# Kernel optimization log

Measured on AMD Instinct MI355X. Metric: run time of the kernel, lower is better.

## Reference

```python
import jax, jax.numpy as jnp
import numpy as np
import math

B, S, D, H = 2, 2048, 1024, 16
DH = D // H  # head_dim = 64


def setup_inputs() -> dict:
    key = jax.random.key(0)
    k0, k1, k2 = jax.random.split(key, 3)
    x = jax.random.normal(k0, (B, S, D), dtype=jnp.float32)
    Wi = jax.random.normal(k1, (3 * D, D), dtype=jnp.float32) * 0.02  # torch (out,in) layout
    bi = jnp.zeros((3 * D,), dtype=jnp.float32)
    Wo = jax.random.normal(k2, (D, D), dtype=jnp.float32) * 0.02
    bo = jnp.zeros((D,), dtype=jnp.float32)
    return {"x": x, "Wi": Wi, "bi": bi, "Wo": Wo, "bo": bo, "causal_mask": 1}


def reference(x, Wi, bi, Wo, bo, causal_mask):
    b, s, d = x.shape
    # fused QKV projection: nn.Linear applies x @ W.T + b
    qkv = x @ Wi.T + bi                      # (b, s, 3d)
    q, k, v = jnp.split(qkv, 3, axis=-1)
    # (b, s, d) -> (b, h, s, dh)
    def to_heads(t):
        return t.reshape(b, s, H, DH).transpose(0, 2, 1, 3)
    q, k, v = to_heads(q), to_heads(k), to_heads(v)
    scores = jnp.einsum("bhqd,bhkd->bhqk", q, k)  # (b, h, s, s)
    if causal_mask:
        # mask strictly-upper triangle with -inf BEFORE scaling (as in source; -inf unaffected)
        tri = jnp.triu(jnp.ones((s, s), dtype=bool), k=1)
        scores = jnp.where(tri, -jnp.inf, scores)
    scores = scores / math.sqrt(DH)
    weight = jax.nn.softmax(scores, axis=-1)
    out = jnp.einsum("bhqk,bhkd->bhqd", weight, v)  # (b, h, s, dh)
    out = out.transpose(0, 2, 1, 3).reshape(b, s, d)
    return out @ Wo.T + bo
```

## Files before the change

### kernel.cpp

```cpp
#include <hip/hip_runtime.h>
#include <hip/hip_bf16.h>
#include <stdint.h>

#define B_    2
#define S_    2048
#define D_    1024
#define H_    16
#define DH_   64
#define MTOT  (B_*S_)
#define NQKV  (3*D_)

typedef __attribute__((ext_vector_type(8))) short  bf16x8;
typedef __attribute__((ext_vector_type(4))) short  bf16x4;
typedef __attribute__((ext_vector_type(4))) float  f32x4;
typedef __attribute__((ext_vector_type(8))) unsigned short u16x8;
typedef unsigned short ushort_t;

__device__ __forceinline__ ushort_t f2bf(float f) {
  union { float f; unsigned int i; } v; v.f = f;
  unsigned int r = v.i + 0x7FFF + ((v.i >> 16) & 1);
  return (ushort_t)(r >> 16);
}

__device__ __forceinline__ unsigned cvt_pk_bf16(float lo, float hi) {
  unsigned r;
  asm("v_cvt_pk_bf16_f32 %0, %1, %2" : "=v"(r) : "v"(lo), "v"(hi));
  return r;
}

__device__ __forceinline__ float fexp2(float x) {
  float r;
  asm("v_exp_f32 %0, %1" : "=v"(r) : "v"(x));
  return r;
}

#if __has_builtin(__builtin_amdgcn_mfma_f32_16x16x16_bf16)
__device__ __forceinline__ f32x4 mfma16(bf16x4 a, bf16x4 b, f32x4 c) {
  return __builtin_amdgcn_mfma_f32_16x16x16_bf16(a, b, c, 0, 0, 0);
}
#elif __has_builtin(__builtin_amdgcn_mfma_f32_16x16x16bf16_1k)
__device__ __forceinline__ f32x4 mfma16(bf16x4 a, bf16x4 b, f32x4 c) {
  return __builtin_amdgcn_mfma_f32_16x16x16bf16_1k(a, b, c, 0, 0, 0);
}
#else
__device__ __forceinline__ f32x4 mfma16(bf16x4 a, bf16x4 b, f32x4 c) {
  asm volatile("v_mfma_f32_16x16x16_bf16 %0, %1, %2, %0"
               : "+v"(c) : "v"(a), "v"(b));
  return c;
}
#endif

__device__ __forceinline__ void gl_lds16(const ushort_t* g, ushort_t* l) {
  __builtin_amdgcn_global_load_lds(
      (const __attribute__((address_space(1))) unsigned int*)g,
      (__attribute__((address_space(3))) unsigned int*)l, 16, 0, 0);
}

#define CVN1 (MTOT*D_/8)
#define CVN2 (NQKV*D_/8)
#define CVN3 (D_*D_/8)
__global__ __launch_bounds__(256) void cvt_all(
    const float* __restrict__ x, const float* __restrict__ Wi, const float* __restrict__ Wo,
    ushort_t* __restrict__ xb, ushort_t* __restrict__ Wib, ushort_t* __restrict__ Wob) {
  int i = blockIdx.x * blockDim.x + threadIdx.x;
  const float* src; ushort_t* dst; int k;
  if (i < CVN1)            { src = x;  dst = xb;  k = i; }
  else if (i < CVN1+CVN2)  { src = Wi; dst = Wib; k = i - CVN1; }
  else                     { src = Wo; dst = Wob; k = i - CVN1 - CVN2; }
  const float4* s4 = (const float4*)src;
  float4 a = s4[2*k], b = s4[2*k+1];
  u16x8 o;
  o[0]=f2bf(a.x); o[1]=f2bf(a.y); o[2]=f2bf(a.z); o[3]=f2bf(a.w);
  o[4]=f2bf(b.x); o[5]=f2bf(b.y); o[6]=f2bf(b.z); o[7]=f2bf(b.w);
  ((u16x8*)dst)[k] = o;
}

#define BKQ 32
#define BKO 64
#define QSCALE 0.18033688011112042f
__global__ __launch_bounds__(256) void gemm_qkv(
    const ushort_t* __restrict__ Abf, const ushort_t* __restrict__ Bbf,
    const float* __restrict__ bias,
    ushort_t* __restrict__ qb, ushort_t* __restrict__ kb, ushort_t* __restrict__ vb) {
  __shared__ __align__(16) ushort_t Al[2][128*BKQ];
  __shared__ __align__(16) ushort_t Bl[2][128*BKQ];
  int tid = threadIdx.x;
  int w = tid >> 6, lane = tid & 63;
  int wrow = (w >> 1) * 64, wcol = (w & 1) * 64;
  int bid = blockIdx.y * 24 + blockIdx.x;
  int swz = (bid & 7) * 96 + (bid >> 3);
  int m0 = (swz / 24) * 128, n0 = (swz % 24) * 128;
  const int K = D_;
  const int nt = K / BKQ;

  auto stageg = [&](int t, int buf) {
    int k0 = t * BKQ;
    #pragma unroll
    for (int it = 0; it < 2; ++it) {
      int c = it*256 + tid;
      int row = c >> 2, cc = c & 3;
      int lbase = (it*256 + w*64) * 8;
      gl_lds16(Abf + (size_t)(m0+row)*K + k0 + cc*8, &Al[buf][lbase]);
      gl_lds16(Bbf + (size_t)(n0+row)*K + k0 + cc*8, &Bl[buf][lbase]);
    }
  };

  f32x4 zero = {0.f, 0.f, 0.f, 0.f};
  f32x4 acc[4][4];
  for (int i=0;i<4;i++) for (int j=0;j<4;j++) acc[i][j] = zero;

  stageg(0, 0);
  asm volatile("s_waitcnt vmcnt(0)" ::: "memory");
  __builtin_amdgcn_s_barrier();

  for (int t = 0; t < nt; ++t) {
    int cur = t & 1;
    if (t + 1 < nt) stageg(t + 1, cur ^ 1);
    int kof = (lane >> 4) * 8;
    bf16x8 af[4], bfr[4];
    for (int i=0;i<4;i++) af[i]  = *(const bf16x8*)(&Al[cur][(wrow + i*16 + (lane&15))*BKQ + kof]);
    for (int j=0;j<4;j++) bfr[j] = *(const bf16x8*)(&Bl[cur][(wcol + j*16 + (lane&15))*BKQ + kof]);
    for (int i=0;i<4;i++)
      for (int j=0;j<4;j++)
        acc[i][j] = __builtin_amdgcn_mfma_f32_16x16x32_bf16(af[i], bfr[j], acc[i][j], 0, 0, 0);
    asm volatile("s_waitcnt vmcnt(0)" ::: "memory");
    __builtin_amdgcn_s_barrier();
  }
  for (int i=0;i<4;i++)
    for (int j=0;j<4;j++)
      for (int r=0;r<4;r++) {
        int gm = m0 + wrow + i*16 + (lane>>4)*4 + r;
        int gn = n0 + wcol + j*16 + (lane&15);
        float v = acc[i][j][r] + bias[gn];
        int b = gm >> 11, s = gm & (S_-1);
        int sect = gn >> 10, hn = gn & (D_-1);
        int hh = hn >> 6, d = hn & 63;
        size_t idx = (((size_t)(b*H_ + hh))*S_ + s)*DH_ + d;
        if (sect == 0) v *= QSCALE;
        ushort_t val = f2bf(v);
        if (sect == 0) qb[idx] = val;
        else if (sect == 1) kb[idx] = val;
        else vb[idx] = val;
      }
}

__global__ __launch_bounds__(256) void transpose_v(
    const ushort_t* __restrict__ vb, ushort_t* __restrict__ vtb) {
  __shared__ ushort_t T[64*72];
  int bh = blockIdx.y;
  int s0 = blockIdx.x * 64;
  int tid = threadIdx.x;
  const ushort_t* src = vb + (size_t)bh * S_ * DH_;
  ushort_t* dst = vtb + (size_t)bh * DH_ * S_;
  for (int it = 0; it < 2; ++it) {
    int c = it*256 + tid;
    int row = c >> 3, cc = c & 7;
    *(uint4*)&T[row*72 + cc*8] = *(const uint4*)(src + (size_t)(s0+row)*DH_ + cc*8);
  }
  __syncthreads();
  for (int it = 0; it < 2; ++it) {
    int c = it*256 + tid;
    int d = c >> 3, sc = c & 7;
    u16x8 o;
    #pragma unroll
    for (int e = 0; e < 8; ++e) o[e] = T[(sc*8+e)*72 + d];
    *(u16x8*)(dst + (size_t)d*S_ + s0 + sc*8) = o;
  }
}

#define KVB 64
#define DTHR 8.0f
__global__ __launch_bounds__(256) void attn_fwd(
    const ushort_t* __restrict__ qb, const ushort_t* __restrict__ kb,
    const ushort_t* __restrict__ vtb, ushort_t* __restrict__ attnb,
    const int* __restrict__ causal) {
  int wg = blockIdx.x;
  int xcd = wg & 7;
  int j = wg >> 3;
  int v = j >> 5;
  int u = j & 31;
  int a = u >> 2;
  int qi = v*8 + ((v & 1) ? (7 - a) : a);
  int qblk = 31 - qi;
  int bh = (u & 3) * 8 + xcd;
  int b = bh >> 4, h = bh & 15;
  int tid = threadIdx.x, w = tid >> 6, lane = tid & 63;
  int g = lane >> 4, q16 = lane & 15;
  const ushort_t* qh  = qb  + (size_t)bh * S_ * DH_;
  const ushort_t* kh  = kb  + (size_t)bh * S_ * DH_;
  const ushort_t* vth = vtb + (size_t)bh * DH_ * S_;
  __shared__ __align__(16) ushort_t Kl[2][KVB*64];
  __shared__ __align__(16) ushort_t Vtl[2][64*KVB];
  bool use_causal = (causal[0] != 0);

  int nkv = use_causal ? (qblk + 1) : (S_/KVB);
  int qw = qblk*64 + w*16;

  bf16x8 qc0 = *(const bf16x8*)(qh + (size_t)(qw + q16)*DH_ +  0 + g*8);
  bf16x8 qc1 = *(const bf16x8*)(qh + (size_t)(qw + q16)*DH_ + 32 + g*8);

  int c0 = tid, c1 = tid + 256;
  int r0 = c0 >> 3, sw0 = ((c0 & 7) ^ (r0 & 7)) * 8;
  int r1 = c1 >> 3, sw1 = ((c1 & 7) ^ (r1 & 7)) * 8;
  const ushort_t* kp0 = kh + r0*DH_ + sw0;
  const ushort_t* kp1 = kh + r1*DH_ + sw1;
  const ushort_t* vp0 = vth + (size_t)r0*S_ + sw0;
  const ushort_t* vp1 = vth + (size_t)r1*S_ + sw1;

  auto stage = [&](int t, int buf) {
    size_t kadv = (size_t)(t*KVB) * DH_;
    int vadv = t*KVB;
    gl_lds16(kp0 + kadv, &Kl[buf][c0*8]);
    gl_lds16(kp1 + kadv, &Kl[buf][c1*8]);
    gl_lds16(vp0 + vadv, &Vtl[buf][c0*8]);
    gl_lds16(vp1 + vadv, &Vtl[buf][c1*8]);
  };

  f32x4 zero = {0.f,0.f,0.f,0.f};
  f32x4 o[4];
  #pragma unroll
  for (int dt=0;dt<4;dt++) o[dt] = zero;
  float mrun = -1e30f, lrun = 0.f;

  stage(0, 0);
  asm volatile("s_waitcnt vmcnt(0)" ::: "memory");
  __builtin_amdgcn_s_barrier();

  for (int it = 0; it < nkv; ++it) {
    int cur = it & 1;
    int kvbase = it * KVB;
    if (it + 1 < nkv) stage(it + 1, cur ^ 1);

    f32x4 sacc[4];
    #pragma unroll
    for (int j2=0;j2<4;j2++) sacc[j2] = zero;
    #pragma unroll
    for (int kk=0;kk<2;kk++) {
      bf16x8 qf = kk ? qc1 : qc0;
      #pragma unroll
      for (int j2=0;j2<4;j2++) {
        int row = j2*16 + q16;
        int slot = (kk*4 + g) ^ (row & 7);
        bf16x8 kf = *(const bf16x8*)(&Kl[cur][row*64 + slot*8]);
        sacc[j2] = __builtin_amdgcn_mfma_f32_16x16x32_bf16(kf, qf, sacc[j2], 0, 0, 0);
      }
    }
    if (use_causal && kvbase + KVB - 1 > qw) {
      int qd = qw + q16 - kvbase;
      #pragma unroll
      for (int j2=0;j2<4;j2++)
        #pragma unroll
        for (int r=0;r<4;r++)
          if (16*j2 + 4*g + r > qd) sacc[j2][r] = -1e30f;
    }
    float m0v = fmaxf(fmaxf(sacc[0][0], sacc[0][1]), fmaxf(sacc[0][2], sacc[0][3]));
    float m1v = fmaxf(fmaxf(sacc[1][0], sacc[1][1]), fmaxf(sacc[1][2], sacc[1][3]));
    float m2v = fmaxf(fmaxf(sacc[2][0], sacc[2][1]), fmaxf(sacc[2][2], sacc[2][3]));
    float m3v = fmaxf(fmaxf(sacc[3][0], sacc[3][1]), fmaxf(sacc[3][2], sacc[3][3]));
    float mx = fmaxf(fmaxf(m0v, m1v), fmaxf(m2v, m3v));
    mx = fmaxf(mx, __shfl_xor(mx, 16, 64));
    mx = fmaxf(mx, __shfl_xor(mx, 32, 64));
    if (!__all(mx - mrun <= DTHR)) {
      float mnew = fmaxf(mrun, mx);
      float alpha = fexp2(mrun - mnew);
      lrun *= alpha;
      float av0 = __shfl(alpha, 4*g + 0, 64);
      float av1 = __shfl(alpha, 4*g + 1, 64);
      float av2 = __shfl(alpha, 4*g + 2, 64);
      float av3 = __shfl(alpha, 4*g + 3, 64);
      #pragma unroll
      for (int dt=0;dt<4;dt++) {
        o[dt][0] *= av0; o[dt][1] *= av1; o[dt][2] *= av2; o[dt][3] *= av3;
      }
      mrun = mnew;
    }
    float p[4][4];
    float rs = 0.f;
    #pragma unroll
    for (int j2=0;j2<4;j2++)
      #pragma unroll
      for (int r=0;r<4;r++) {
        p[j2][r] = fexp2(sacc[j2][r] - mrun);
        rs += p[j2][r];
      }
    rs += __shfl_xor(rs, 16, 64);
    rs += __shfl_xor(rs, 32, 64);
    lrun += rs;
    #pragma unroll
    for (int s=0;s<4;s++) {
      union { unsigned u2[2]; bf16x4 v2; } pk;
      pk.u2[0] = cvt_pk_bf16(p[s][0], p[s][1]);
      pk.u2[1] = cvt_pk_bf16(p[s][2], p[s][3]);
      int E = 16*s + 4*g;
      #pragma unroll
      for (int dt=0;dt<4;dt++) {
        int row = dt*16 + q16;
        int off = row*64 + ((E >> 3) ^ (row & 7))*8 + (E & 7);
        bf16x4 vf = *(const bf16x4*)(&Vtl[cur][off]);
        o[dt] = mfma16(pk.v2, vf, o[dt]);
      }
    }
    asm volatile("s_waitcnt vmcnt(0)" ::: "memory");
    __builtin_amdgcn_s_barrier();
  }
  float li0 = 1.f / __shfl(lrun, 4*g + 0, 64);
  float li1 = 1.f / __shfl(lrun, 4*g + 1, 64);
  float li2 = 1.f / __shfl(lrun, 4*g + 2, 64);
  float li3 = 1.f / __shfl(lrun, 4*g + 3, 64);
  #pragma unroll
  for (int r=0;r<4;r++) {
    float li = (r==0)?li0:(r==1)?li1:(r==2)?li2:li3;
    int q = qw + 4*g + r;
    #pragma unroll
    for (int dt=0;dt<4;dt++) {
      int d = dt*16 + q16;
      attnb[((size_t)(b*S_ + q))*D_ + h*DH_ + d] = f2bf(o[dt][r] * li);
    }
  }
}

__global__ __launch_bounds__(512) void gemm_out(
    const ushort_t* __restrict__ Abf, const ushort_t* __restrict__ Bbf,
    const float* __restrict__ bias, float* __restrict__ out) {
  __shared__ __align__(16) ushort_t Al[2][128*BKO];
  __shared__ __align__(16) ushort_t Bl[2][128*BKO];
  int tid = threadIdx.x;
  int w = tid >> 6, lane = tid & 63;
  int g = lane >> 4, q16 = lane & 15;
  int wrow = (w >> 2) * 64, wcol = (w & 3) * 32;
  int m0 = blockIdx.y * 128, n0 = blockIdx.x * 128;
  const int K = D_;
  const int nt = K / BKO;

  auto stageg = [&](int t, int buf) {
    int k0 = t * BKO;
    #pragma unroll
    for (int it = 0; it < 2; ++it) {
      int c = it*512 + tid;
      int row = c >> 3, scc = ((c & 7) ^ (row & 7)) * 8;
      gl_lds16(Abf + (size_t)(m0+row)*K + k0 + scc, &Al[buf][c*8]);
      gl_lds16(Bbf + (size_t)(n0+row)*K + k0 + scc, &Bl[buf][c*8]);
    }
  };

  f32x4 zero = {0.f,0.f,0.f,0.f};
  f32x4 acc[4][2];
  for (int i=0;i<4;i++) for (int j=0;j<2;j++) acc[i][j] = zero;

  stageg(0, 0);
  asm volatile("s_waitcnt vmcnt(0)" ::: "memory");
  __builtin_amdgcn_s_barrier();

  for (int t = 0; t < nt; ++t) {
    int cur = t & 1;
    if (t + 1 < nt) stageg(t + 1, cur ^ 1);
    #pragma unroll
    for (int kk = 0; kk < 2; ++kk) {
      bf16x8 af[4], bfr[2];
      #pragma unroll
      for (int i=0;i<4;i++) {
        int row = wrow + i*16 + q16;
        int slot = ((kk*4 + g) ^ (row & 7)) * 8;
        af[i] = *(const bf16x8*)(&Al[cur][row*BKO + slot]);
      }
      #pragma unroll
      for (int j=0;j<2;j++) {
        int row = wcol + j*16 + q16;
        int slot = ((kk*4 + g) ^ (row & 7)) * 8;
        bfr[j] = *(const bf16x8*)(&Bl[cur][row*BKO + slot]);
      }
      #pragma unroll
      for (int i=0;i<4;i++)
        #pragma unroll
        for (int j=0;j<2;j++)
          acc[i][j] = __builtin_amdgcn_mfma_f32_16x16x32_bf16(af[i], bfr[j], acc[i][j], 0, 0, 0);
    }
    asm volatile("s_waitcnt vmcnt(0)" ::: "memory");
    __builtin_amdgcn_s_barrier();
  }
  #pragma unroll
  for (int i=0;i<4;i++)
    #pragma unroll
    for (int j=0;j<2;j++)
      #pragma unroll
      for (int r=0;r<4;r++) {
        int gm = m0 + wrow + i*16 + g*4 + r;
        int gn = n0 + wcol + j*16 + q16;
        out[(size_t)gm*D_ + gn] = acc[i][j][r] + bias[gn];
      }
}

extern "C" void kernel_launch(void* const* d_in, const int* in_sizes, int n_in,
                              void* d_out, int out_size, void* d_ws, size_t ws_size,
                              hipStream_t stream) {
  const float* x  = (const float*)d_in[0];
  const float* Wi = (const float*)d_in[1];
  const float* bi = (const float*)d_in[2];
  const float* Wo = (const float*)d_in[3];
  const float* bo = (const float*)d_in[4];
  const int* causal = (const int*)d_in[5];
  float* out = (float*)d_out;

  ushort_t* xb   = (ushort_t*)d_ws;
  ushort_t* Wib  = xb  + (size_t)MTOT*D_;
  ushort_t* Wob  = Wib + (size_t)NQKV*D_;
  ushort_t* qbuf = Wob + (size_t)D_*D_;
  ushort_t* kbuf = qbuf + (size_t)B_*H_*S_*DH_;
  ushort_t* vbuf = kbuf + (size_t)B_*H_*S_*DH_;
  ushort_t* attnb = vbuf + (size_t)B_*H_*S_*DH_;
  ushort_t* vtb  = xb;

  int ntot = CVN1 + CVN2 + CVN3;
  cvt_all<<<(ntot+255)/256, 256, 0, stream>>>(x, Wi, Wo, xb, Wib, Wob);

  gemm_qkv<<<dim3(NQKV/128, MTOT/128), 256, 0, stream>>>(xb, Wib, bi, qbuf, kbuf, vbuf);
  transpose_v<<<dim3(S_/64, B_*H_), 256, 0, stream>>>(vbuf, vtb);
  attn_fwd<<<1024, 256, 0, stream>>>(qbuf, kbuf, vtb, attnb, causal);
  gemm_out<<<dim3(D_/128, MTOT/128), 512, 0, stream>>>(attnb, Wob, bo, out);
}
```

Baseline: 119.6 us.

## Process two 16-row query tiles per wave in attention to reuse K/V fragments

```diff
diff --git a/kernel.cpp b/kernel.cpp
--- a/kernel.cpp
+++ b/kernel.cpp
@@ -170,7 +170,7 @@
 
 #define KVB 64
 #define DTHR 8.0f
-__global__ __launch_bounds__(256) void attn_fwd(
+__global__ __launch_bounds__(128) void attn_fwd(
     const ushort_t* __restrict__ qb, const ushort_t* __restrict__ kb,
     const ushort_t* __restrict__ vtb, ushort_t* __restrict__ attnb,
     const int* __restrict__ causal) {
@@ -194,33 +194,41 @@
   bool use_causal = (causal[0] != 0);
 
   int nkv = use_causal ? (qblk + 1) : (S_/KVB);
-  int qw = qblk*64 + w*16;
-
-  bf16x8 qc0 = *(const bf16x8*)(qh + (size_t)(qw + q16)*DH_ +  0 + g*8);
-  bf16x8 qc1 = *(const bf16x8*)(qh + (size_t)(qw + q16)*DH_ + 32 + g*8);
-
-  int c0 = tid, c1 = tid + 256;
-  int r0 = c0 >> 3, sw0 = ((c0 & 7) ^ (r0 & 7)) * 8;
-  int r1 = c1 >> 3, sw1 = ((c1 & 7) ^ (r1 & 7)) * 8;
-  const ushort_t* kp0 = kh + r0*DH_ + sw0;
-  const ushort_t* kp1 = kh + r1*DH_ + sw1;
-  const ushort_t* vp0 = vth + (size_t)r0*S_ + sw0;
-  const ushort_t* vp1 = vth + (size_t)r1*S_ + sw1;
-
+  int qw = qblk*64 + w*32;
+
+  bf16x8 qc[2][2];
+  #pragma unroll
+  for (int qt=0; qt<2; ++qt)
+    #pragma unroll
+    for (int kk=0; kk<2; ++kk)
+      qc[qt][kk] = *(const bf16x8*)(qh + (size_t)(qw + qt*16 + q16)*DH_ + kk*32 + g*8);
+
+  const ushort_t* kp[4]; const ushort_t* vp[4]; int ldo[4];
+  #pragma unroll
+  for (int k2=0;k2<4;k2++) {
+    int c = tid + k2*128;
+    int row = c >> 3, sw = ((c & 7) ^ (row & 7)) * 8;
+    kp[k2] = kh + row*DH_ + sw;
+    vp[k2] = vth + (size_t)row*S_ + sw;
+    ldo[k2] = c*8;
+  }
   auto stage = [&](int t, int buf) {
     size_t kadv = (size_t)(t*KVB) * DH_;
     int vadv = t*KVB;
-    gl_lds16(kp0 + kadv, &Kl[buf][c0*8]);
-    gl_lds16(kp1 + kadv, &Kl[buf][c1*8]);
-    gl_lds16(vp0 + vadv, &Vtl[buf][c0*8]);
-    gl_lds16(vp1 + vadv, &Vtl[buf][c1*8]);
+    #pragma unroll
+    for (int k2=0;k2<4;k2++) {
+      gl_lds16(kp[k2] + kadv, &Kl[buf][ldo[k2]]);
+      gl_lds16(vp[k2] + vadv, &Vtl[buf][ldo[k2]]);
+    }
   };
 
   f32x4 zero = {0.f,0.f,0.f,0.f};
-  f32x4 o[4];
+  f32x4 o[2][4];
   #pragma unroll
-  for (int dt=0;dt<4;dt++) o[dt] = zero;
-  float mrun = -1e30f, lrun = 0.f;
+  for (int qt=0;qt<2;qt++)
+    #pragma unroll
+    for (int dt=0;dt<4;dt++) o[qt][dt] = zero;
+  float mrun[2] = {-1e30f, -1e30f}, lrun[2] = {0.f, 0.f};
 
   stage(0, 0);
   asm volatile("s_waitcnt vmcnt(0)" ::: "memory");
@@ -231,90 +239,110 @@
     int kvbase = it * KVB;
     if (it + 1 < nkv) stage(it + 1, cur ^ 1);
 
-    f32x4 sacc[4];
-    #pragma unroll
-    for (int j2=0;j2<4;j2++) sacc[j2] = zero;
-    #pragma unroll
-    for (int kk=0;kk<2;kk++) {
-      bf16x8 qf = kk ? qc1 : qc0;
+    bf16x8 kf[2][4];
+    #pragma unroll
+    for (int kk=0;kk<2;kk++)
       #pragma unroll
       for (int j2=0;j2<4;j2++) {
         int row = j2*16 + q16;
         int slot = (kk*4 + g) ^ (row & 7);
-        bf16x8 kf = *(const bf16x8*)(&Kl[cur][row*64 + slot*8]);
-        sacc[j2] = __builtin_amdgcn_mfma_f32_16x16x32_bf16(kf, qf, sacc[j2], 0, 0, 0);
-      }
-    }
-    if (use_causal && kvbase + KVB - 1 > qw) {
-      int qd = qw + q16 - kvbase;
+        kf[kk][j2] = *(const bf16x8*)(&Kl[cur][row*64 + slot*8]);
+      }
+    f32x4 sacc[2][4];
+    #pragma unroll
+    for (int qt=0;qt<2;qt++)
+      #pragma unroll
+      for (int j2=0;j2<4;j2++) sacc[qt][j2] = zero;
+    #pragma unroll
+    for (int qt=0;qt<2;qt++)
+      #pragma unroll
+      for (int kk=0;kk<2;kk++)
+        #pragma unroll
+        for (int j2=0;j2<4;j2++)
+          sacc[qt][j2] = __builtin_amdgcn_mfma_f32_16x16x32_bf16(kf[kk][j2], qc[qt][kk], sacc[qt][j2], 0, 0, 0);
+
+    bf16x4 pkv[2][4];
+    #pragma unroll
+    for (int qt=0;qt<2;qt++) {
+      if (use_causal && kvbase + KVB - 1 > qw + qt*16) {
+        int qd = qw + qt*16 + q16 - kvbase;
+        #pragma unroll
+        for (int j2=0;j2<4;j2++)
+          #pragma unroll
+          for (int r=0;r<4;r++)
+            if (16*j2 + 4*g + r > qd) sacc[qt][j2][r] = -1e30f;
+      }
+      float m0v = fmaxf(fmaxf(sacc[qt][0][0], sacc[qt][0][1]), fmaxf(sacc[qt][0][2], sacc[qt][0][3]));
+      float m1v = fmaxf(fmaxf(sacc[qt][1][0], sacc[qt][1][1]), fmaxf(sacc[qt][1][2], sacc[qt][1][3]));
+      float m2v = fmaxf(fmaxf(sacc[qt][2][0], sacc[qt][2][1]), fmaxf(sacc[qt][2][2], sacc[qt][2][3]));
+      float m3v = fmaxf(fmaxf(sacc[qt][3][0], sacc[qt][3][1]), fmaxf(sacc[qt][3][2], sacc[qt][3][3]));
+      float mx = fmaxf(fmaxf(m0v, m1v), fmaxf(m2v, m3v));
+      mx = fmaxf(mx, __shfl_xor(mx, 16, 64));
+      mx = fmaxf(mx, __shfl_xor(mx, 32, 64));
+      if (!__all(mx - mrun[qt] <= DTHR)) {
+        float mnew = fmaxf(mrun[qt], mx);
+        float alpha = fexp2(mrun[qt] - mnew);
+        lrun[qt] *= alpha;
+        float av0 = __shfl(alpha, 4*g + 0, 64);
+        float av1 = __shfl(alpha, 4*g + 1, 64);
+        float av2 = __shfl(alpha, 4*g + 2, 64);
+        float av3 = __shfl(alpha, 4*g + 3, 64);
+        #pragma unroll
+        for (int dt=0;dt<4;dt++) {
+          o[qt][dt][0] *= av0; o[qt][dt][1] *= av1; o[qt][dt][2] *= av2; o[qt][dt][3] *= av3;
+        }
+        mrun[qt] = mnew;
+      }
+      float p[4][4];
+      float rs = 0.f;
       #pragma unroll
       for (int j2=0;j2<4;j2++)
         #pragma unroll
-        for (int r=0;r<4;r++)
-          if (16*j2 + 4*g + r > qd) sacc[j2][r] = -1e30f;
-    }
-    float m0v = fmaxf(fmaxf(sacc[0][0], sacc[0][1]), fmaxf(sacc[0][2], sacc[0][3]));
-    float m1v = fmaxf(fmaxf(sacc[1][0], sacc[1][1]), fmaxf(sacc[1][2], sacc[1][3]));
-    float m2v = fmaxf(fmaxf(sacc[2][0], sacc[2][1]), fmaxf(sacc[2][2], sacc[2][3]));
-    float m3v = fmaxf(fmaxf(sacc[3][0], sacc[3][1]), fmaxf(sacc[3][2], sacc[3][3]));
-    float mx = fmaxf(fmaxf(m0v, m1v), fmaxf(m2v, m3v));
-    mx = fmaxf(mx, __shfl_xor(mx, 16, 64));
-    mx = fmaxf(mx, __shfl_xor(mx, 32, 64));
-    if (!__all(mx - mrun <= DTHR)) {
-      float mnew = fmaxf(mrun, mx);
-      float alpha = fexp2(mrun - mnew);
-      lrun *= alpha;
-      float av0 = __shfl(alpha, 4*g + 0, 64);
-      float av1 = __shfl(alpha, 4*g + 1, 64);
-      float av2 = __shfl(alpha, 4*g + 2, 64);
-      float av3 = __shfl(alpha, 4*g + 3, 64);
-      #pragma unroll
-      for (int dt=0;dt<4;dt++) {
-        o[dt][0] *= av0; o[dt][1] *= av1; o[dt][2] *= av2; o[dt][3] *= av3;
-      }
-      mrun = mnew;
-    }
-    float p[4][4];
-    float rs = 0.f;
-    #pragma unroll
-    for (int j2=0;j2<4;j2++)
-      #pragma unroll
-      for (int r=0;r<4;r++) {
-        p[j2][r] = fexp2(sacc[j2][r] - mrun);
-        rs += p[j2][r];
-      }
-    rs += __shfl_xor(rs, 16, 64);
-    rs += __shfl_xor(rs, 32, 64);
-    lrun += rs;
+        for (int r=0;r<4;r++) {
+          p[j2][r] = fexp2(sacc[qt][j2][r] - mrun[qt]);
+          rs += p[j2][r];
+        }
+      rs += __shfl_xor(rs, 16, 64);
+      rs += __shfl_xor(rs, 32, 64);
+      lrun[qt] += rs;
+      #pragma unroll
+      for (int s=0;s<4;s++) {
+        union { unsigned u2[2]; bf16x4 v2; } pk;
+        pk.u2[0] = cvt_pk_bf16(p[s][0], p[s][1]);
+        pk.u2[1] = cvt_pk_bf16(p[s][2], p[s][3]);
+        pkv[qt][s] = pk.v2;
+      }
+    }
     #pragma unroll
     for (int s=0;s<4;s++) {
-      union { unsigned u2[2]; bf16x4 v2; } pk;
-      pk.u2[0] = cvt_pk_bf16(p[s][0], p[s][1]);
-      pk.u2[1] = cvt_pk_bf16(p[s][2], p[s][3]);
       int E = 16*s + 4*g;
       #pragma unroll
       for (int dt=0;dt<4;dt++) {
         int row = dt*16 + q16;
         int off = row*64 + ((E >> 3) ^ (row & 7))*8 + (E & 7);
         bf16x4 vf = *(const bf16x4*)(&Vtl[cur][off]);
-        o[dt] = mfma16(pk.v2, vf, o[dt]);
+        o[0][dt] = mfma16(pkv[0][s], vf, o[0][dt]);
+        o[1][dt] = mfma16(pkv[1][s], vf, o[1][dt]);
       }
     }
     asm volatile("s_waitcnt vmcnt(0)" ::: "memory");
     __builtin_amdgcn_s_barrier();
   }
-  float li0 = 1.f / __shfl(lrun, 4*g + 0, 64);
-  float li1 = 1.f / __shfl(lrun, 4*g + 1, 64);
-  float li2 = 1.f / __shfl(lrun, 4*g + 2, 64);
-  float li3 = 1.f / __shfl(lrun, 4*g + 3, 64);
   #pragma unroll
-  for (int r=0;r<4;r++) {
-    float li = (r==0)?li0:(r==1)?li1:(r==2)?li2:li3;
-    int q = qw + 4*g + r;
-    #pragma unroll
-    for (int dt=0;dt<4;dt++) {
-      int d = dt*16 + q16;
-      attnb[((size_t)(b*S_ + q))*D_ + h*DH_ + d] = f2bf(o[dt][r] * li);
+  for (int qt=0;qt<2;qt++) {
+    float li0 = 1.f / __shfl(lrun[qt], 4*g + 0, 64);
+    float li1 = 1.f / __shfl(lrun[qt], 4*g + 1, 64);
+    float li2 = 1.f / __shfl(lrun[qt], 4*g + 2, 64);
+    float li3 = 1.f / __shfl(lrun[qt], 4*g + 3, 64);
+    #pragma unroll
+    for (int r=0;r<4;r++) {
+      float li = (r==0)?li0:(r==1)?li1:(r==2)?li2:li3;
+      int q = qw + qt*16 + 4*g + r;
+      #pragma unroll
+      for (int dt=0;dt<4;dt++) {
+        int d = dt*16 + q16;
+        attnb[((size_t)(b*S_ + q))*D_ + h*DH_ + d] = f2bf(o[qt][dt][r] * li);
+      }
     }
   }
 }
@@ -415,6 +443,6 @@
 
   gemm_qkv<<<dim3(NQKV/128, MTOT/128), 256, 0, stream>>>(xb, Wib, bi, qbuf, kbuf, vbuf);
   transpose_v<<<dim3(S_/64, B_*H_), 256, 0, stream>>>(vbuf, vtb);
-  attn_fwd<<<1024, 256, 0, stream>>>(qbuf, kbuf, vtb, attnb, causal);
+  attn_fwd<<<1024, 128, 0, stream>>>(qbuf, kbuf, vtb, attnb, causal);
   gemm_out<<<dim3(D_/128, MTOT/128), 512, 0, stream>>>(attnb, Wob, bo, out);
 }
```

Measured after the change: 131.1 us. +9.6%, slower.

## Restructure QKV GEMM with 512 threads, BK=64 and XOR-swizzled LDS

Applied to the files above, without the earlier changes.

```diff
diff --git a/kernel.cpp b/kernel.cpp
--- a/kernel.cpp
+++ b/kernel.cpp
@@ -75,39 +75,38 @@
   ((u16x8*)dst)[k] = o;
 }
 
-#define BKQ 32
 #define BKO 64
 #define QSCALE 0.18033688011112042f
-__global__ __launch_bounds__(256) void gemm_qkv(
+__global__ __launch_bounds__(512) void gemm_qkv(
     const ushort_t* __restrict__ Abf, const ushort_t* __restrict__ Bbf,
     const float* __restrict__ bias,
     ushort_t* __restrict__ qb, ushort_t* __restrict__ kb, ushort_t* __restrict__ vb) {
-  __shared__ __align__(16) ushort_t Al[2][128*BKQ];
-  __shared__ __align__(16) ushort_t Bl[2][128*BKQ];
+  __shared__ __align__(16) ushort_t Al[2][128*BKO];
+  __shared__ __align__(16) ushort_t Bl[2][128*BKO];
   int tid = threadIdx.x;
   int w = tid >> 6, lane = tid & 63;
-  int wrow = (w >> 1) * 64, wcol = (w & 1) * 64;
+  int g = lane >> 4, q16 = lane & 15;
+  int wrow = (w >> 2) * 64, wcol = (w & 3) * 32;
   int bid = blockIdx.y * 24 + blockIdx.x;
   int swz = (bid & 7) * 96 + (bid >> 3);
   int m0 = (swz / 24) * 128, n0 = (swz % 24) * 128;
   const int K = D_;
-  const int nt = K / BKQ;
+  const int nt = K / BKO;
 
   auto stageg = [&](int t, int buf) {
-    int k0 = t * BKQ;
+    int k0 = t * BKO;
     #pragma unroll
     for (int it = 0; it < 2; ++it) {
-      int c = it*256 + tid;
-      int row = c >> 2, cc = c & 3;
-      int lbase = (it*256 + w*64) * 8;
-      gl_lds16(Abf + (size_t)(m0+row)*K + k0 + cc*8, &Al[buf][lbase]);
-      gl_lds16(Bbf + (size_t)(n0+row)*K + k0 + cc*8, &Bl[buf][lbase]);
+      int c = it*512 + tid;
+      int row = c >> 3, scc = ((c & 7) ^ (row & 7)) * 8;
+      gl_lds16(Abf + (size_t)(m0+row)*K + k0 + scc, &Al[buf][c*8]);
+      gl_lds16(Bbf + (size_t)(n0+row)*K + k0 + scc, &Bl[buf][c*8]);
     }
   };
 
-  f32x4 zero = {0.f, 0.f, 0.f, 0.f};
-  f32x4 acc[4][4];
-  for (int i=0;i<4;i++) for (int j=0;j<4;j++) acc[i][j] = zero;
+  f32x4 zero = {0.f,0.f,0.f,0.f};
+  f32x4 acc[4][2];
+  for (int i=0;i<4;i++) for (int j=0;j<2;j++) acc[i][j] = zero;
 
   stageg(0, 0);
   asm volatile("s_waitcnt vmcnt(0)" ::: "memory");
@@ -116,21 +115,38 @@
   for (int t = 0; t < nt; ++t) {
     int cur = t & 1;
     if (t + 1 < nt) stageg(t + 1, cur ^ 1);
-    int kof = (lane >> 4) * 8;
-    bf16x8 af[4], bfr[4];
-    for (int i=0;i<4;i++) af[i]  = *(const bf16x8*)(&Al[cur][(wrow + i*16 + (lane&15))*BKQ + kof]);
-    for (int j=0;j<4;j++) bfr[j] = *(const bf16x8*)(&Bl[cur][(wcol + j*16 + (lane&15))*BKQ + kof]);
-    for (int i=0;i<4;i++)
-      for (int j=0;j<4;j++)
-        acc[i][j] = __builtin_amdgcn_mfma_f32_16x16x32_bf16(af[i], bfr[j], acc[i][j], 0, 0, 0);
+    #pragma unroll
+    for (int kk = 0; kk < 2; ++kk) {
+      bf16x8 af[4], bfr[2];
+      #pragma unroll
+      for (int i=0;i<4;i++) {
+        int row = wrow + i*16 + q16;
+        int slot = ((kk*4 + g) ^ (row & 7)) * 8;
+        af[i] = *(const bf16x8*)(&Al[cur][row*BKO + slot]);
+      }
+      #pragma unroll
+      for (int j=0;j<2;j++) {
+        int row = wcol + j*16 + q16;
+        int slot = ((kk*4 + g) ^ (row & 7)) * 8;
+        bfr[j] = *(const bf16x8*)(&Bl[cur][row*BKO + slot]);
+      }
+      #pragma unroll
+      for (int i=0;i<4;i++)
+        #pragma unroll
+        for (int j=0;j<2;j++)
+          acc[i][j] = __builtin_amdgcn_mfma_f32_16x16x32_bf16(af[i], bfr[j], acc[i][j], 0, 0, 0);
+    }
     asm volatile("s_waitcnt vmcnt(0)" ::: "memory");
     __builtin_amdgcn_s_barrier();
   }
+  #pragma unroll
   for (int i=0;i<4;i++)
-    for (int j=0;j<4;j++)
+    #pragma unroll
+    for (int j=0;j<2;j++)
+      #pragma unroll
       for (int r=0;r<4;r++) {
-        int gm = m0 + wrow + i*16 + (lane>>4)*4 + r;
-        int gn = n0 + wcol + j*16 + (lane&15);
+        int gm = m0 + wrow + i*16 + g*4 + r;
+        int gn = n0 + wcol + j*16 + q16;
         float v = acc[i][j][r] + bias[gn];
         int b = gm >> 11, s = gm & (S_-1);
         int sect = gn >> 10, hn = gn & (D_-1);
@@ -413,7 +429,7 @@
   int ntot = CVN1 + CVN2 + CVN3;
   cvt_all<<<(ntot+255)/256, 256, 0, stream>>>(x, Wi, Wo, xb, Wib, Wob);
 
-  gemm_qkv<<<dim3(NQKV/128, MTOT/128), 256, 0, stream>>>(xb, Wib, bi, qbuf, kbuf, vbuf);
+  gemm_qkv<<<dim3(NQKV/128, MTOT/128), 512, 0, stream>>>(xb, Wib, bi, qbuf, kbuf, vbuf);
   transpose_v<<<dim3(S_/64, B_*H_), 256, 0, stream>>>(vbuf, vtb);
   attn_fwd<<<1024, 256, 0, stream>>>(qbuf, kbuf, vtb, attnb, causal);
   gemm_out<<<dim3(D_/128, MTOT/128), 512, 0, stream>>>(attnb, Wob, bo, out);
```

Result: faster. 114.4 us (-4.4%).
